# Kernel optimization log

Measured on AMD Instinct MI355X. Metric: run time of the kernel, lower is better.

The kernel has to match this reference:

```python
import jax, jax.numpy as jnp
import numpy as np

NZ = 128
N_GEN = 8
BATCH = 2048
SLOPE = 0.2


def _convt(x, w, b, stride, pad):
    # PyTorch ConvTranspose2d(weight [Cin,Cout,kH,kW], stride, padding p)
    # == conv with lhs_dilation=stride, padding=k-1-p, spatially-flipped
    # kernel with in/out channels swapped.
    k = jnp.flip(w, axis=(2, 3)).transpose(2, 3, 0, 1)  # [kH,kW,Cin,Cout]
    y = jax.lax.conv_general_dilated(
        x, k, window_strides=(1, 1), padding=[(pad, pad), (pad, pad)],
        lhs_dilation=(stride, stride),
        dimension_numbers=('NCHW', 'HWIO', 'NCHW'))
    return y + b[None, :, None, None]


def setup_inputs() -> dict:
    key = jax.random.key(0)
    ks = jax.random.split(key, 12)
    s = 0.05
    return {
        'z': jax.random.normal(ks[0], (BATCH, NZ), jnp.float32),
        'g_idx': jax.random.randint(ks[1], (BATCH,), 0, N_GEN),
        'W1': jax.random.normal(ks[2], (N_GEN, NZ, 256), jnp.float32) * s,
        'b1': jax.random.normal(ks[3], (N_GEN, 256), jnp.float32) * s,
        'W2': jax.random.normal(ks[4], (N_GEN, 256, 1568), jnp.float32) * s,
        'b2': jax.random.normal(ks[5], (N_GEN, 1568), jnp.float32) * s,
        'cw1': jax.random.normal(ks[6], (N_GEN, 32, 16, 4, 4), jnp.float32) * s,
        'cb1': jax.random.normal(ks[7], (N_GEN, 16), jnp.float32) * s,
        'cw2': jax.random.normal(ks[8], (N_GEN, 16, 8, 4, 4), jnp.float32) * s,
        'cb2': jax.random.normal(ks[9], (N_GEN, 8), jnp.float32) * s,
        'cw3': jax.random.normal(ks[10], (N_GEN, 8, 1, 3, 3), jnp.float32) * s,
        'cb3': jax.random.normal(ks[11], (N_GEN, 1), jnp.float32) * s,
    }


def _single_gen(params, z):
    W1, b1, W2, b2, cw1, cb1, cw2, cb2, cw3, cb3 = params
    lrelu = lambda x: jax.nn.leaky_relu(x, SLOPE)
    h = lrelu(z @ W1 + b1)                 # [B,256]
    h = lrelu(h @ W2 + b2)                 # [B,1568]
    h = h.reshape(-1, 32, 7, 7)
    h = lrelu(_convt(h, cw1, cb1, 2, 2))   # [B,16,14,14]
    h = lrelu(_convt(h, cw2, cb2, 2, 2))   # [B,8,28,28]
    return jnp.tanh(_convt(h, cw3, cb3, 1, 1))  # [B,1,28,28]


def reference(z, g_idx, W1, b1, W2, b2, cw1, cb1, cw2, cb2, cw3, cb3):
    params = (W1, b1, W2, b2, cw1, cb1, cw2, cb2, cw3, cb3)
    # Compute every generator on the full batch (faithful to the torch loop),
    # vmapped over the generator axis: images [G,B,1,28,28].
    images = jax.vmap(_single_gen, in_axes=((0,) * 10, None))(params, z)
    # Per-sample gather: keep generator g_idx[b] for each sample b.
    return images[g_idx, jnp.arange(z.shape[0])]
```

## Files before the change

### kernel.cpp

```cpp
#include <hip/hip_runtime.h>
#include <cstdint>
#include <cstddef>

#define BATCH 2048
#define NZ 128
#define NGEN 8
#define GRPS 32
#define MAXG 72
#define NCT 13
#define H2_ELEMS 1792
#define WS_H1_OFF 16384
#define WS_H2_OFF (16384 + MAXG * 8192 * 4)
#define WS_W2T_OFF (WS_H2_OFF + BATCH * H2_ELEMS * 2)
#define W2T_GSTRIDE (1568 * 256)
#define NB_W2T (NGEN * 49)
#define NB_PREP (NB_W2T + MAXG * 4)
#define WS_WPK1_OFF (WS_W2T_OFF + NGEN * W2T_GSTRIDE * 2)
#define WS_WPK2_OFF (WS_WPK1_OFF + NGEN * 4096 * 4)
#define WS_WPK3_OFF (WS_WPK2_OFF + NGEN * 1024 * 4)
#define PS 168

typedef unsigned int u32;
typedef unsigned short u16;
typedef unsigned long long u64;
typedef _Float16 f16x8 __attribute__((ext_vector_type(8)));
typedef _Float16 f16x4 __attribute__((ext_vector_type(4)));
typedef _Float16 f16x2 __attribute__((ext_vector_type(2)));
typedef float f32x4 __attribute__((ext_vector_type(4)));

__device__ __forceinline__ float lrelu(float x) { return fmaxf(x, 0.2f * x); }
__device__ __forceinline__ u16 f16b(float f) {
    _Float16 h = (_Float16)f;
    return __builtin_bit_cast(u16, h);
}
__device__ __forceinline__ u32 pk2(float a, float b) {
    f16x2 v; v[0] = (_Float16)a; v[1] = (_Float16)b;
    return __builtin_bit_cast(u32, v);
}
__device__ __forceinline__ float dot2(u32 a, u32 b, float c) {
#if __has_builtin(__builtin_amdgcn_fdot2)
    return __builtin_amdgcn_fdot2(__builtin_bit_cast(f16x2, a),
                                  __builtin_bit_cast(f16x2, b), c, false);
#else
    float d;
    asm("v_dot2_f32_f16 %0, %1, %2, %3" : "=v"(d) : "v"(a), "v"(b), "v"(c));
    return d;
#endif
}
__device__ __forceinline__ float fast_tanh(float x) {
    x = fminf(fmaxf(x, -9.f), 9.f);
    const float e = __expf(2.f * x);
    return (e - 1.f) / (e + 1.f);
}
__device__ __forceinline__ int h2off(int n) {
    const int ci = n / 49, rm = n % 49;
    return ci * 56 + (rm / 7) * 8 + (rm % 7);
}

__global__ void bin_kernel(const int* __restrict__ g_idx, int* __restrict__ wsi) {
    __shared__ int wcnt[4][NGEN];
    __shared__ int wboff[4][NGEN];
    __shared__ int pbase[NGEN + 1];
    __shared__ u16 rank[BATCH];
    const int tid = threadIdx.x;
    const int w = tid >> 6, lane = tid & 63;
    if (tid < 4 * NGEN) wcnt[tid >> 3][tid & 7] = 0;
    __syncthreads();
    const u64 lt = ((u64)1 << lane) - 1;
    #pragma unroll
    for (int r = 0; r < 8; ++r) {
        const int b = r * 256 + tid;
        const int gg = g_idx[b];
        u64 m[NGEN];
        #pragma unroll
        for (int k = 0; k < NGEN; ++k) m[k] = __ballot(gg == k);
        rank[b] = (u16)((int)__popcll(m[gg] & lt) + wcnt[w][gg]);
        if (lane < NGEN) wcnt[w][lane] += (int)__popcll(m[lane]);
    }
    __syncthreads();
    if (tid == 0) {
        int acc = 0;
        for (int g = 0; g < NGEN; ++g) {
            pbase[g] = acc;
            const int tot = wcnt[0][g] + wcnt[1][g] + wcnt[2][g] + wcnt[3][g];
            acc += ((tot + GRPS - 1) / GRPS) * GRPS;
        }
        pbase[NGEN] = acc;
        wsi[0] = acc;
    }
    __syncthreads();
    if (tid < 32) {
        const int ww = tid >> 3, g = tid & 7;
        int off = pbase[g];
        for (int w2 = 0; w2 < ww; ++w2) off += wcnt[w2][g];
        wboff[ww][g] = off;
    }
    const int total = pbase[NGEN];
    for (int i = tid; i < total; i += 256) wsi[16 + i] = -1;
    __syncthreads();
    #pragma unroll
    for (int r = 0; r < 8; ++r) {
        const int b = r * 256 + tid;
        const int gg = g_idx[b];
        wsi[16 + wboff[w][gg] + (int)rank[b]] = b;
    }
}

__global__ __launch_bounds__(256) void prep_kernel(
    const float* __restrict__ z, const int* __restrict__ g_idx,
    const float* __restrict__ W1, const float* __restrict__ b1,
    const float* __restrict__ W2, const int* __restrict__ wsi,
    float* __restrict__ h1g, _Float16* __restrict__ W2T,
    const float* __restrict__ cw1, const float* __restrict__ cw2,
    const float* __restrict__ cw3,
    u32* __restrict__ wpk1, u32* __restrict__ wpk2, u32* __restrict__ wpk3)
{
    __shared__ _Float16 t[32][264];
    __shared__ float zst[NZ][12];
    __shared__ int sb[8];
    __shared__ int sG;

    const int tid = threadIdx.x;
    const int bx = blockIdx.x;

    if (bx >= NB_PREP) {
        const int g = bx - NB_PREP;
        const float* c1p = cw1 + g * 8192;
        u32* o1 = wpk1 + g * 4096;
        for (int i = tid; i < 4096; i += 256) {
            const int cip = i >> 8, a = (i >> 6) & 3, co = (i >> 2) & 15, c = i & 3;
            const float* s = c1p + cip * 512 + co * 16 + a * 4 + c;
            o1[i] = pk2(s[0], s[256]);
        }
        const float* c2p = cw2 + g * 2048;
        u32* o2 = wpk2 + g * 1024;
        for (int i = tid; i < 1024; i += 256) {
            const int cip = i >> 7, a = (i >> 5) & 3, co = (i >> 2) & 7, c = i & 3;
            const float* s = c2p + cip * 256 + co * 16 + a * 4 + c;
            o2[i] = pk2(s[0], s[128]);
        }
        if (tid < 36) {
            const int cip = tid / 9, r = tid % 9;
            const float* s = cw3 + g * 72 + cip * 18 + r;
            wpk3[g * 36 + tid] = pk2(s[0], s[9]);
        }
        return;
    }

    if (bx < NB_W2T) {
        const int g = bx / 49;
        const int n0 = (bx % 49) * 32;
        const float* src = W2 + (size_t)g * 256 * 1568;
        const int nl = tid & 31, kh = tid >> 5;
        #pragma unroll 8
        for (int p = 0; p < 32; ++p) {
            const int k = p * 8 + kh;
            t[nl][k] = (_Float16)src[(size_t)k * 1568 + n0 + nl];
        }
        __syncthreads();
        _Float16* dst = W2T + (size_t)g * W2T_GSTRIDE + (size_t)n0 * 256;
        #pragma unroll
        for (int ii = 0; ii < 4; ++ii) {
            const int i = tid + 256 * ii;
            const int n = i >> 5, kc = i & 31;
            *(uint4*)(dst + (size_t)n * 256 + kc * 8) = *(const uint4*)&t[n][kc * 8];
        }
        return;
    }

    const int bx2 = bx - NB_W2T;
    const int grp = bx2 >> 2;
    const int s0 = (bx2 & 3) * 8;
    if (grp * GRPS >= wsi[0]) return;

    if (tid == 0) sG = g_idx[wsi[16 + grp * GRPS]];
    if (tid < 8) sb[tid] = wsi[16 + grp * GRPS + s0 + tid];
    __syncthreads();
    const float* W1g = W1 + sG * (NZ * 256);
    const float* b1g = b1 + sG * 256;

    {
        const int s = tid >> 5, f = tid & 31;
        float4 v = make_float4(0.f, 0.f, 0.f, 0.f);
        if (sb[s] >= 0) v = *(const float4*)(z + (size_t)sb[s] * NZ + 4 * f);
        zst[4 * f + 0][s] = v.x; zst[4 * f + 1][s] = v.y;
        zst[4 * f + 2][s] = v.z; zst[4 * f + 3][s] = v.w;
    }
    __syncthreads();

    const int c = tid;
    float acc[8];
    #pragma unroll
    for (int s = 0; s < 8; ++s) acc[s] = 0.f;
    const float* wp = W1g + c;
    #pragma unroll 4
    for (int k = 0; k < NZ; ++k) {
        const float w = wp[k * 256];
        float av[8];
        *(float4*)&av[0] = *(const float4*)&zst[k][0];
        *(float4*)&av[4] = *(const float4*)&zst[k][4];
        #pragma unroll
        for (int s = 0; s < 8; ++s) acc[s] += av[s] * w;
    }
    const float bv = b1g[c];
    float* hp = h1g + (size_t)grp * 8192 + (size_t)s0 * 256 + c;
    #pragma unroll
    for (int s = 0; s < 8; ++s) hp[s * 256] = lrelu(acc[s] + bv);
}

__global__ __launch_bounds__(256) void fc2_kernel(
    const int* __restrict__ g_idx,
    const _Float16* __restrict__ W2T, const float* __restrict__ b2,
    const int* __restrict__ wsi, const float* __restrict__ h1g,
    u16* __restrict__ h2g)
{
    __shared__ __align__(16) char afsm[16384];
    _Float16* afrag = (_Float16*)afsm;
    __shared__ int sb[GRPS];
    __shared__ int sG;

    const int tid = threadIdx.x;
    const int grp = blockIdx.x / NCT;
    const int tile = blockIdx.x % NCT;
    if (grp * GRPS >= wsi[0]) return;

    if (tid == 0) sG = g_idx[wsi[16 + grp * GRPS]];
    if (tid < GRPS) sb[tid] = wsi[16 + grp * GRPS + tid];
    __syncthreads();
    const _Float16* W2Tg = W2T + (size_t)sG * W2T_GSTRIDE;
    const float* b2g = b2 + sG * 1568;

    {
        const float4* h1p4 = (const float4*)(h1g + (size_t)grp * 8192);
        #pragma unroll
        for (int i = 0; i < 8; ++i) {
            const int u = tid + 256 * i;
            const int j4 = u & 1;
            const int ln = (u >> 1) & 63;
            const int kq = (u >> 7) & 7;
            const int mt = (u >> 10) & 1;
            const int s = mt * 16 + (ln & 15);
            const float4 v = h1p4[s * 64 + kq * 8 + ((ln >> 4) << 1) + j4];
            f16x4 hi;
            hi[0] = (_Float16)v.x; hi[1] = (_Float16)v.y;
            hi[2] = (_Float16)v.z; hi[3] = (_Float16)v.w;
            const int bh = ((mt * 8 + kq) * 64 + ln) * 8 + 4 * j4;
            *(f16x4*)&afrag[bh] = hi;
        }
    }
    __syncthreads();

    const int wave = tid >> 6;
    const int lane = tid & 63;
    const int q = lane >> 4;
    const int nl = lane & 15;
    const int nb0 = tile * 128 + 2 * wave * 16;
    const int nb1 = nb0 + 16;
    const bool act0 = nb0 < 1568, act1 = nb1 < 1568;

    f32x4 accA0 = {0.f, 0.f, 0.f, 0.f}, accB0 = accA0;
    f32x4 accA1 = accA0, accB1 = accA0;
    if (act0) {
        const _Float16* bp = W2Tg + (size_t)(nb0 + nl) * 256 + q * 8;
        #pragma unroll
        for (int kq = 0; kq < 8; ++kq) {
            const f16x8 b = *(const f16x8*)(bp + kq * 32);
            const f16x8 a0 = *(const f16x8*)&afrag[((0 * 8 + kq) * 64 + lane) * 8];
            const f16x8 a1 = *(const f16x8*)&afrag[((1 * 8 + kq) * 64 + lane) * 8];
            accA0 = __builtin_amdgcn_mfma_f32_16x16x32_f16(a0, b, accA0, 0, 0, 0);
            accB0 = __builtin_amdgcn_mfma_f32_16x16x32_f16(a1, b, accB0, 0, 0, 0);
        }
    }
    if (act1) {
        const _Float16* bp = W2Tg + (size_t)(nb1 + nl) * 256 + q * 8;
        #pragma unroll
        for (int kq = 0; kq < 8; ++kq) {
            const f16x8 b = *(const f16x8*)(bp + kq * 32);
            const f16x8 a0 = *(const f16x8*)&afrag[((0 * 8 + kq) * 64 + lane) * 8];
            const f16x8 a1 = *(const f16x8*)&afrag[((1 * 8 + kq) * 64 + lane) * 8];
            accA1 = __builtin_amdgcn_mfma_f32_16x16x32_f16(a0, b, accA1, 0, 0, 0);
            accB1 = __builtin_amdgcn_mfma_f32_16x16x32_f16(a1, b, accB1, 0, 0, 0);
        }
    }
    __syncthreads();

    u16* pst = (u16*)afsm;
    const int nstart = tile * 128;
    const int nend = (nstart + 128 < 1568) ? nstart + 128 : 1568;
    const int offLo = h2off(nstart), offHi = h2off(nend - 1);
    const int lo8 = offLo & ~7;

    if (act0) {
        const int n = nb0 + nl;
        const float bias = b2g[n];
        u16* pp = pst + (h2off(n) - lo8);
        #pragma unroll
        for (int reg = 0; reg < 4; ++reg) {
            pp[(q * 4 + reg) * PS]        = f16b(lrelu(accA0[reg] + bias));
            pp[(16 + q * 4 + reg) * PS]   = f16b(lrelu(accB0[reg] + bias));
        }
    }
    if (act1) {
        const int n = nb1 + nl;
        const float bias = b2g[n];
        u16* pp = pst + (h2off(n) - lo8);
        #pragma unroll
        for (int reg = 0; reg < 4; ++reg) {
            pp[(q * 4 + reg) * PS]        = f16b(lrelu(accA1[reg] + bias));
            pp[(16 + q * 4 + reg) * PS]   = f16b(lrelu(accB1[reg] + bias));
        }
    }
    __syncthreads();

    {
        const int s = tid >> 3, p = tid & 7;
        const int bb = sb[s];
        if (bb >= 0) {
            u16* row = h2g + (size_t)bb * H2_ELEMS;
            const u16* ps = pst + s * PS - lo8;
            const int c0 = (offLo + 7) & ~7;
            const int c1 = (offHi + 1) & ~7;
            for (int o = offLo + p; o < c0 && o <= offHi; o += 8) row[o] = ps[o];
            const int t0 = (c1 > offLo) ? c1 : offLo;
            for (int o = t0 + p; o <= offHi; o += 8) row[o] = ps[o];
            for (int c = c0 + p * 8; c + 8 <= c1; c += 64)
                *(uint4*)(row + c) = *(const uint4*)(ps + c);
        }
    }
}

template <int H>
__device__ __forceinline__ void conv2p_half(
    const u32 (*c1s)[14][20], u16* dst,
    const u32* __restrict__ w2g, const float bv, const int co, const int y)
{
    float acc[14];
    #pragma unroll
    for (int xx = 0; xx < 14; ++xx) acc[xx] = bv;
    const int a0 = (y + 1) & 1;
    for (int aa = 0; aa < 2; ++aa) {
        const int a = a0 + 2 * aa;
        const int iy = (y + 1 - a) >> 1;
        if ((unsigned)iy < 14u) {
            #pragma unroll 2
            for (int cip = 0; cip < 8; ++cip) {
                u32 rr[10];
                if (H == 0) {
                    *(uint4*)&rr[0] = *(const uint4*)&c1s[cip][iy][0];
                    *(uint4*)&rr[4] = *(const uint4*)&c1s[cip][iy][4];
                } else {
                    *(uint4*)&rr[0] = *(const uint4*)&c1s[cip][iy][4];
                    *(uint4*)&rr[4] = *(const uint4*)&c1s[cip][iy][8];
                    *(uint2*)&rr[8] = *(const uint2*)&c1s[cip][iy][12];
                }
                const uint4 wq = *(const uint4*)(w2g + ((cip * 4 + a) * 8 + co) * 4);
                const u32 wv[4] = {wq.x, wq.y, wq.z, wq.w};
                #pragma unroll
                for (int xx = 0; xx < 14; ++xx) {
                    const int x = 14 * H + xx;
                    const int c0v = (x + 1) & 1;
                    const int ix0 = (x + 1 - c0v) >> 1;
                    const int li = ix0 - 4 * H;
                    if (ix0 < 14) acc[xx] = dot2(rr[li],     wv[c0v],     acc[xx]);
                    if (ix0 >= 1) acc[xx] = dot2(rr[li - 1], wv[c0v + 2], acc[xx]);
                }
            }
        }
    }
    #pragma unroll
    for (int xx = 0; xx < 14; ++xx) dst[2 * (14 * H + xx)] = f16b(lrelu(acc[xx]));
}

__global__ __launch_bounds__(256, 6) void conv_kernel(
    const int* __restrict__ g_idx,
    const u32* __restrict__ wpk1, const float* __restrict__ cb1,
    const u32* __restrict__ wpk2, const float* __restrict__ cb2,
    const u32* __restrict__ wpk3, const float* __restrict__ cb3,
    const u16* __restrict__ h2g, float* __restrict__ out)
{
    __shared__ __align__(16) char smem[8960 + 14784];
    u32 (*c1s)[14][20] = (u32 (*)[14][20])smem;
    u32 (*h2s)[7][8]   = (u32 (*)[7][8])(smem + 8960);
    u32 (*c2s)[28][33] = (u32 (*)[28][33])(smem + 8960);
    __shared__ u32 w3s[36];

    const int tid = threadIdx.x;
    const int b = blockIdx.x;
    const int g = g_idx[b];
    const u32* w1g = wpk1 + g * 4096;
    const u32* w2g = wpk2 + g * 1024;
    const float* cb1g = cb1 + g * 16;
    const float* cb2g = cb2 + g * 8;
    const float  cb3v = cb3[g];

    if (tid < 224) {
        const uint4 qv = ((const uint4*)(h2g + (size_t)b * H2_ELEMS))[tid];
        const int ci = tid / 7, yq = tid % 7;
        u16* dst = (u16*)&h2s[ci >> 1][yq][0] + (ci & 1);
        const u32 w[4] = {qv.x, qv.y, qv.z, qv.w};
        #pragma unroll
        for (int j = 0; j < 4; ++j) {
            dst[4 * j]     = (u16)(w[j] & 0xffffu);
            dst[4 * j + 2] = (u16)(w[j] >> 16);
        }
    }
    if (tid < 36) w3s[tid] = wpk3[g * 36 + tid];
    __syncthreads();

    if (tid < 224) {
        const int co = tid / 14, y = tid % 14;
        const float bv = cb1g[co];
        float acc[14];
        #pragma unroll
        for (int x = 0; x < 14; ++x) acc[x] = bv;
        const int a0 = (y + 1) & 1;
        for (int aa = 0; aa < 2; ++aa) {
            const int a = a0 + 2 * aa;
            const int iy = (y + 1 - a) >> 1;
            if ((unsigned)iy < 7u) {
                #pragma unroll 2
                for (int cip = 0; cip < 16; ++cip) {
                    u32 rr[8];
                    *(uint4*)&rr[0] = *(const uint4*)&h2s[cip][iy][0];
                    *(uint4*)&rr[4] = *(const uint4*)&h2s[cip][iy][4];
                    const uint4 wq = *(const uint4*)(w1g + ((cip * 4 + a) * 16 + co) * 4);
                    const u32 wv[4] = {wq.x, wq.y, wq.z, wq.w};
                    #pragma unroll
                    for (int x = 0; x < 14; ++x) {
                        const int c0v = (x + 1) & 1;
                        const int ix0 = (x + 1 - c0v) >> 1;
                        if (ix0 < 7)  acc[x] = dot2(rr[ix0],     wv[c0v],     acc[x]);
                        if (ix0 >= 1) acc[x] = dot2(rr[ix0 - 1], wv[c0v + 2], acc[x]);
                    }
                }
            }
        }
        u16* dst = (u16*)&c1s[co >> 1][y][0] + (co & 1);
        #pragma unroll
        for (int x = 0; x < 14; ++x) dst[2 * x] = f16b(lrelu(acc[x]));
    }
    __syncthreads();

    if (tid < 224) {
        const int co = tid / 28, y = tid % 28;
        const float bv = cb2g[co];
        u16* dst = (u16*)&c2s[co >> 1][y][0] + (co & 1);
        conv2p_half<0>(c1s, dst, w2g, bv, co, y);
        conv2p_half<1>(c1s, dst, w2g, bv, co, y);
    }
    __syncthreads();

    if (tid < 196) {
        const int y = tid / 7, qq = tid % 7;
        const int xb = qq * 4;
        float acc[4] = {cb3v, cb3v, cb3v, cb3v};
        #pragma unroll 2
        for (int cip = 0; cip < 4; ++cip) {
            u32 wp[9];
            #pragma unroll
            for (int j = 0; j < 9; ++j) wp[j] = w3s[cip * 9 + j];
            #pragma unroll
            for (int a = 0; a < 3; ++a) {
                const int iy = y + 1 - a;
                if ((unsigned)iy < 28u) {
                    u32 rr[6];
                    #pragma unroll
                    for (int j = 0; j < 6; ++j) {
                        const int ix = xb - 1 + j;
                        rr[j] = ((unsigned)ix < 28u) ? c2s[cip][iy][ix] : 0u;
                    }
                    #pragma unroll
                    for (int xx = 0; xx < 4; ++xx)
                        #pragma unroll
                        for (int c = 0; c < 3; ++c)
                            acc[xx] = dot2(rr[xx + 2 - c], wp[a * 3 + c], acc[xx]);
                }
            }
        }
        float* op = out + (size_t)b * 784 + y * 28 + xb;
        #pragma unroll
        for (int xx = 0; xx < 4; ++xx) op[xx] = fast_tanh(acc[xx]);
    }
}

extern "C" void kernel_launch(void* const* d_in, const int* in_sizes, int n_in,
                              void* d_out, int out_size, void* d_ws, size_t ws_size,
                              hipStream_t stream) {
    const float* z   = (const float*)d_in[0];
    const int*   gi  = (const int*)d_in[1];
    const float* W1  = (const float*)d_in[2];
    const float* b1  = (const float*)d_in[3];
    const float* W2  = (const float*)d_in[4];
    const float* b2  = (const float*)d_in[5];
    const float* cw1 = (const float*)d_in[6];
    const float* cb1 = (const float*)d_in[7];
    const float* cw2 = (const float*)d_in[8];
    const float* cb2 = (const float*)d_in[9];
    const float* cw3 = (const float*)d_in[10];
    const float* cb3 = (const float*)d_in[11];
    int*      wsi = (int*)d_ws;
    float*    h1g = (float*)((char*)d_ws + WS_H1_OFF);
    u16*      h2g = (u16*)((char*)d_ws + WS_H2_OFF);
    _Float16* w2t = (_Float16*)((char*)d_ws + WS_W2T_OFF);
    u32*      wpk1 = (u32*)((char*)d_ws + WS_WPK1_OFF);
    u32*      wpk2 = (u32*)((char*)d_ws + WS_WPK2_OFF);
    u32*      wpk3 = (u32*)((char*)d_ws + WS_WPK3_OFF);

    bin_kernel<<<1, 256, 0, stream>>>(gi, wsi);
    prep_kernel<<<NB_PREP + NGEN, 256, 0, stream>>>(z, gi, W1, b1, W2, wsi, h1g, w2t,
                                                    cw1, cw2, cw3, wpk1, wpk2, wpk3);
    fc2_kernel<<<MAXG * NCT, 256, 0, stream>>>(gi, w2t, b2, wsi, h1g, h2g);
    conv_kernel<<<BATCH, 256, 0, stream>>>(gi, wpk1, cb1, wpk2, cb2, wpk3, cb3,
                                           h2g, (float*)d_out);
}
```

Before: 161.2 us.

## Fold sample binning into prep kernel and run conv blocks in generator-sorted order

Removes the single-block bin_kernel launch. Each fc1 block in prep_kernel now recomputes the per-generator ranks and offsets itself, and one extra block writes the sorted index list to the workspace. This removes a serial kernel-boundary dependency, at the cost of redundant ballot and popcount work in every fc1 block. conv_kernel now indexes samples through the sorted list, so consecutive blocks share generator weights, but it launches padded slots that return early. It also raises the unroll factor on two conv inner loops.

```diff
diff --git a/kernel.cpp b/kernel.cpp
--- a/kernel.cpp
+++ b/kernel.cpp
@@ -57,97 +57,22 @@
     return ci * 56 + (rm / 7) * 8 + (rm % 7);
 }
 
-__global__ void bin_kernel(const int* __restrict__ g_idx, int* __restrict__ wsi) {
-    __shared__ int wcnt[4][NGEN];
-    __shared__ int wboff[4][NGEN];
-    __shared__ int pbase[NGEN + 1];
-    __shared__ u16 rank[BATCH];
-    const int tid = threadIdx.x;
-    const int w = tid >> 6, lane = tid & 63;
-    if (tid < 4 * NGEN) wcnt[tid >> 3][tid & 7] = 0;
-    __syncthreads();
-    const u64 lt = ((u64)1 << lane) - 1;
-    #pragma unroll
-    for (int r = 0; r < 8; ++r) {
-        const int b = r * 256 + tid;
-        const int gg = g_idx[b];
-        u64 m[NGEN];
-        #pragma unroll
-        for (int k = 0; k < NGEN; ++k) m[k] = __ballot(gg == k);
-        rank[b] = (u16)((int)__popcll(m[gg] & lt) + wcnt[w][gg]);
-        if (lane < NGEN) wcnt[w][lane] += (int)__popcll(m[lane]);
-    }
-    __syncthreads();
-    if (tid == 0) {
-        int acc = 0;
-        for (int g = 0; g < NGEN; ++g) {
-            pbase[g] = acc;
-            const int tot = wcnt[0][g] + wcnt[1][g] + wcnt[2][g] + wcnt[3][g];
-            acc += ((tot + GRPS - 1) / GRPS) * GRPS;
-        }
-        pbase[NGEN] = acc;
-        wsi[0] = acc;
-    }
-    __syncthreads();
-    if (tid < 32) {
-        const int ww = tid >> 3, g = tid & 7;
-        int off = pbase[g];
-        for (int w2 = 0; w2 < ww; ++w2) off += wcnt[w2][g];
-        wboff[ww][g] = off;
-    }
-    const int total = pbase[NGEN];
-    for (int i = tid; i < total; i += 256) wsi[16 + i] = -1;
-    __syncthreads();
-    #pragma unroll
-    for (int r = 0; r < 8; ++r) {
-        const int b = r * 256 + tid;
-        const int gg = g_idx[b];
-        wsi[16 + wboff[w][gg] + (int)rank[b]] = b;
-    }
-}
-
 __global__ __launch_bounds__(256) void prep_kernel(
     const float* __restrict__ z, const int* __restrict__ g_idx,
     const float* __restrict__ W1, const float* __restrict__ b1,
-    const float* __restrict__ W2, const int* __restrict__ wsi,
+    const float* __restrict__ W2, int* __restrict__ wsi,
     float* __restrict__ h1g, _Float16* __restrict__ W2T,
     const float* __restrict__ cw1, const float* __restrict__ cw2,
     const float* __restrict__ cw3,
     u32* __restrict__ wpk1, u32* __restrict__ wpk2, u32* __restrict__ wpk3)
 {
-    __shared__ _Float16 t[32][264];
-    __shared__ float zst[NZ][12];
-    __shared__ int sb[8];
-    __shared__ int sG;
+    __shared__ __align__(16) char pmem[16896];
 
     const int tid = threadIdx.x;
     const int bx = blockIdx.x;
 
-    if (bx >= NB_PREP) {
-        const int g = bx - NB_PREP;
-        const float* c1p = cw1 + g * 8192;
-        u32* o1 = wpk1 + g * 4096;
-        for (int i = tid; i < 4096; i += 256) {
-            const int cip = i >> 8, a = (i >> 6) & 3, co = (i >> 2) & 15, c = i & 3;
-            const float* s = c1p + cip * 512 + co * 16 + a * 4 + c;
-            o1[i] = pk2(s[0], s[256]);
-        }
-        const float* c2p = cw2 + g * 2048;
-        u32* o2 = wpk2 + g * 1024;
-        for (int i = tid; i < 1024; i += 256) {
-            const int cip = i >> 7, a = (i >> 5) & 3, co = (i >> 2) & 7, c = i & 3;
-            const float* s = c2p + cip * 256 + co * 16 + a * 4 + c;
-            o2[i] = pk2(s[0], s[128]);
-        }
-        if (tid < 36) {
-            const int cip = tid / 9, r = tid % 9;
-            const float* s = cw3 + g * 72 + cip * 18 + r;
-            wpk3[g * 36 + tid] = pk2(s[0], s[9]);
-        }
-        return;
-    }
-
     if (bx < NB_W2T) {
+        _Float16 (*t)[264] = (_Float16 (*)[264])pmem;
         const int g = bx / 49;
         const int n0 = (bx % 49) * 32;
         const float* src = W2 + (size_t)g * 256 * 1568;
@@ -168,16 +93,105 @@
         return;
     }
 
+    if (bx >= NB_PREP && bx < NB_PREP + NGEN) {
+        const int g = bx - NB_PREP;
+        const float* c1p = cw1 + g * 8192;
+        u32* o1 = wpk1 + g * 4096;
+        for (int i = tid; i < 4096; i += 256) {
+            const int cip = i >> 8, a = (i >> 6) & 3, co = (i >> 2) & 15, c = i & 3;
+            const float* s = c1p + cip * 512 + co * 16 + a * 4 + c;
+            o1[i] = pk2(s[0], s[256]);
+        }
+        const float* c2p = cw2 + g * 2048;
+        u32* o2 = wpk2 + g * 1024;
+        for (int i = tid; i < 1024; i += 256) {
+            const int cip = i >> 7, a = (i >> 5) & 3, co = (i >> 2) & 7, c = i & 3;
+            const float* s = c2p + cip * 256 + co * 16 + a * 4 + c;
+            o2[i] = pk2(s[0], s[128]);
+        }
+        if (tid < 36) {
+            const int cip = tid / 9, r = tid % 9;
+            const float* s = cw3 + g * 72 + cip * 18 + r;
+            wpk3[g * 36 + tid] = pk2(s[0], s[9]);
+        }
+        return;
+    }
+
+    u16* rank       = (u16*)pmem;
+    int (*wcnt)[NGEN]  = (int (*)[NGEN])(pmem + 4096);
+    int (*wboff)[NGEN] = (int (*)[NGEN])(pmem + 4224);
+    int* pbase      = (int*)(pmem + 4352);
+    const int w = tid >> 6, lane = tid & 63;
+    if (tid < 4 * NGEN) wcnt[tid >> 3][tid & 7] = 0;
+    __syncthreads();
+    const u64 lt = ((u64)1 << lane) - 1;
+    #pragma unroll
+    for (int r = 0; r < 8; ++r) {
+        const int b = r * 256 + tid;
+        const int gg = g_idx[b];
+        u64 m[NGEN];
+        #pragma unroll
+        for (int k = 0; k < NGEN; ++k) m[k] = __ballot(gg == k);
+        rank[b] = (u16)((int)__popcll(m[gg] & lt) + wcnt[w][gg]);
+        if (lane < NGEN) wcnt[w][lane] += (int)__popcll(m[lane]);
+    }
+    __syncthreads();
+    if (tid == 0) {
+        int acc = 0;
+        for (int g = 0; g < NGEN; ++g) {
+            pbase[g] = acc;
+            const int tot = wcnt[0][g] + wcnt[1][g] + wcnt[2][g] + wcnt[3][g];
+            acc += ((tot + GRPS - 1) / GRPS) * GRPS;
+        }
+        pbase[NGEN] = acc;
+    }
+    __syncthreads();
+    if (tid < 32) {
+        const int ww = tid >> 3, g = tid & 7;
+        int off = pbase[g];
+        for (int w2 = 0; w2 < ww; ++w2) off += wcnt[w2][g];
+        wboff[ww][g] = off;
+    }
+    __syncthreads();
+
+    if (bx >= NB_PREP + NGEN) {
+        if (tid == 0) wsi[0] = pbase[NGEN];
+        for (int i = tid; i < MAXG * GRPS; i += 256) wsi[16 + i] = -1;
+        __syncthreads();
+        #pragma unroll
+        for (int r = 0; r < 8; ++r) {
+            const int b = r * 256 + tid;
+            const int gg = g_idx[b];
+            wsi[16 + wboff[w][gg] + (int)rank[b]] = b;
+        }
+        return;
+    }
+
     const int bx2 = bx - NB_W2T;
     const int grp = bx2 >> 2;
     const int s0 = (bx2 & 3) * 8;
-    if (grp * GRPS >= wsi[0]) return;
-
-    if (tid == 0) sG = g_idx[wsi[16 + grp * GRPS]];
-    if (tid < 8) sb[tid] = wsi[16 + grp * GRPS + s0 + tid];
-    __syncthreads();
-    const float* W1g = W1 + sG * (NZ * 256);
-    const float* b1g = b1 + sG * 256;
+    if (grp * GRPS >= pbase[NGEN]) return;
+
+    int gsel = 0;
+    #pragma unroll
+    for (int g = 1; g < NGEN; ++g) if (grp * GRPS >= pbase[g]) gsel = g;
+
+    int* sb = (int*)(pmem + 4400);
+    float (*zst)[12] = (float (*)[12])(pmem + 4608);
+    if (tid < 8) sb[tid] = -1;
+    __syncthreads();
+    const int base = grp * GRPS + s0;
+    #pragma unroll
+    for (int r = 0; r < 8; ++r) {
+        const int b = r * 256 + tid;
+        const int gg = g_idx[b];
+        const int rel = wboff[w][gg] + (int)rank[b] - base;
+        if ((unsigned)rel < 8u) sb[rel] = b;
+    }
+    __syncthreads();
+
+    const float* W1g = W1 + gsel * (NZ * 256);
+    const float* b1g = b1 + gsel * 256;
 
     {
         const int s = tid >> 5, f = tid & 31;
@@ -195,12 +209,12 @@
     const float* wp = W1g + c;
     #pragma unroll 4
     for (int k = 0; k < NZ; ++k) {
-        const float w = wp[k * 256];
+        const float wv = wp[k * 256];
         float av[8];
         *(float4*)&av[0] = *(const float4*)&zst[k][0];
         *(float4*)&av[4] = *(const float4*)&zst[k][4];
         #pragma unroll
-        for (int s = 0; s < 8; ++s) acc[s] += av[s] * w;
+        for (int s = 0; s < 8; ++s) acc[s] += av[s] * wv;
     }
     const float bv = b1g[c];
     float* hp = h1g + (size_t)grp * 8192 + (size_t)s0 * 256 + c;
@@ -342,7 +356,7 @@
         const int a = a0 + 2 * aa;
         const int iy = (y + 1 - a) >> 1;
         if ((unsigned)iy < 14u) {
-            #pragma unroll 2
+            #pragma unroll 4
             for (int cip = 0; cip < 8; ++cip) {
                 u32 rr[10];
                 if (H == 0) {
@@ -372,7 +386,7 @@
 }
 
 __global__ __launch_bounds__(256, 6) void conv_kernel(
-    const int* __restrict__ g_idx,
+    const int* __restrict__ g_idx, const int* __restrict__ wsi,
     const u32* __restrict__ wpk1, const float* __restrict__ cb1,
     const u32* __restrict__ wpk2, const float* __restrict__ cb2,
     const u32* __restrict__ wpk3, const float* __restrict__ cb3,
@@ -385,7 +399,8 @@
     __shared__ u32 w3s[36];
 
     const int tid = threadIdx.x;
-    const int b = blockIdx.x;
+    const int b = wsi[16 + blockIdx.x];
+    if (b < 0) return;
     const int g = g_idx[b];
     const u32* w1g = wpk1 + g * 4096;
     const u32* w2g = wpk2 + g * 1024;
@@ -418,7 +433,7 @@
             const int a = a0 + 2 * aa;
             const int iy = (y + 1 - a) >> 1;
             if ((unsigned)iy < 7u) {
-                #pragma unroll 2
+                #pragma unroll 4
                 for (int cip = 0; cip < 16; ++cip) {
                     u32 rr[8];
                     *(uint4*)&rr[0] = *(const uint4*)&h2s[cip][iy][0];
@@ -506,10 +521,10 @@
     u32*      wpk2 = (u32*)((char*)d_ws + WS_WPK2_OFF);
     u32*      wpk3 = (u32*)((char*)d_ws + WS_WPK3_OFF);
 
-    bin_kernel<<<1, 256, 0, stream>>>(gi, wsi);
-    prep_kernel<<<NB_PREP + NGEN, 256, 0, stream>>>(z, gi, W1, b1, W2, wsi, h1g, w2t,
-                                                    cw1, cw2, cw3, wpk1, wpk2, wpk3);
+    prep_kernel<<<NB_PREP + NGEN + 1, 256, 0, stream>>>(z, gi, W1, b1, W2, wsi,
+                                                        h1g, w2t, cw1, cw2, cw3,
+                                                        wpk1, wpk2, wpk3);
     fc2_kernel<<<MAXG * NCT, 256, 0, stream>>>(gi, w2t, b2, wsi, h1g, h2g);
-    conv_kernel<<<BATCH, 256, 0, stream>>>(gi, wpk1, cb1, wpk2, cb2, wpk3, cb3,
-                                           h2g, (float*)d_out);
-}
+    conv_kernel<<<MAXG * GRPS, 256, 0, stream>>>(gi, wsi, wpk1, cb1, wpk2, cb2,
+                                                 wpk3, cb3, h2g, (float*)d_out);
+}
```

Result: no change. 163.9 us (+1.7%).
